# Kernel optimization log

Measured on AMD Instinct MI355X. Metric: run time of the kernel, lower is better.

The kernel has to match this reference:

```python
import jax, jax.numpy as jnp
import numpy as np

B, T, D = 2, 2048, 2048
HQ, HKV, HD = 16, 8, 128
GROUP = HQ // HKV
EPS = 1e-6


def rms_norm(x, scale):
    # qwen3-compatible: compute in fp32
    xf = x.astype(jnp.float32)
    var = jnp.mean(xf * xf, axis=-1, keepdims=True)
    return (xf * jax.lax.rsqrt(var + EPS) * scale).astype(x.dtype)


def apply_rope(x, cos, sin):
    # x: [B,H,T,d]; cos,sin: [T,d]
    d2 = x.shape[-1] // 2
    x1, x2 = x[..., :d2], x[..., d2:]
    rot = jnp.concatenate([-x2, x1], axis=-1)
    return (x * cos[None, None] + rot * sin[None, None]).astype(x.dtype)


def setup_inputs() -> dict:
    key = jax.random.key(0)
    ks = jax.random.split(key, 8)
    x = jax.random.normal(ks[0], (B, T, D), dtype=jnp.float32)
    # causal mask: True where attention is disallowed (j > i)
    mask = jnp.triu(jnp.ones((T, T), dtype=jnp.bool_), k=1)
    # RoPE tables
    inv_freq = 1.0 / (10000.0 ** (np.arange(0, HD, 2, dtype=np.float32) / HD))
    pos = np.arange(T, dtype=np.float32)
    ang = np.outer(pos, inv_freq)  # [T, HD/2]
    ang = np.concatenate([ang, ang], axis=-1)  # [T, HD]
    cos = jnp.asarray(np.cos(ang), dtype=jnp.float32)
    sin = jnp.asarray(np.sin(ang), dtype=jnp.float32)
    s = 0.02
    Wq = jax.random.normal(ks[1], (HQ * HD, D), dtype=jnp.float32) * s
    Wk = jax.random.normal(ks[2], (HKV * HD, D), dtype=jnp.float32) * s
    Wv = jax.random.normal(ks[3], (HKV * HD, D), dtype=jnp.float32) * s
    Wo = jax.random.normal(ks[4], (D, HQ * HD), dtype=jnp.float32) * s
    q_scale = jnp.ones((HD,), dtype=jnp.float32)
    k_scale = jnp.ones((HD,), dtype=jnp.float32)
    return {"x": x, "mask": mask, "cos": cos, "sin": sin,
            "Wq": Wq, "Wk": Wk, "Wv": Wv, "Wo": Wo,
            "q_scale": q_scale, "k_scale": k_scale}


def reference(x, mask, cos, sin, Wq, Wk, Wv, Wo, q_scale, k_scale):
    Bc, Tc, _ = x.shape
    Q = jnp.einsum('btd,ed->bte', x, Wq).reshape(Bc, Tc, HQ, HD).transpose(0, 2, 1, 3)
    K = jnp.einsum('btd,ed->bte', x, Wk).reshape(Bc, Tc, HKV, HD).transpose(0, 2, 1, 3)
    V = jnp.einsum('btd,ed->bte', x, Wv).reshape(Bc, Tc, HKV, HD).transpose(0, 2, 1, 3)
    Q = rms_norm(Q, q_scale)
    K = rms_norm(K, k_scale)
    Q = apply_rope(Q, cos, sin)
    K = apply_rope(K, cos, sin)
    K = jnp.repeat(K, GROUP, axis=1)  # [B,HQ,T,d]
    V = jnp.repeat(V, GROUP, axis=1)
    S = jnp.einsum('bhqd,bhkd->bhqk', Q, K) / jnp.sqrt(jnp.float32(HD))
    S = jnp.where(mask[None, None], -jnp.inf, S)
    P = jax.nn.softmax(S, axis=-1)
    ctx = jnp.einsum('bhqk,bhkd->bhqd', P, V).transpose(0, 2, 1, 3).reshape(Bc, Tc, HQ * HD)
    return jnp.einsum('bte,de->btd', ctx, Wo)
```

## Files before the change

kernel.cpp:

```cpp
#include <hip/hip_runtime.h>
#include <cstdint>
#include <cstddef>

#define B_ 2
#define T_ 2048
#define D_ 2048
#define HQ_ 16
#define HKV_ 8
#define HD_ 128

typedef __attribute__((ext_vector_type(8))) short short8;
typedef __attribute__((ext_vector_type(8))) unsigned short ushort8;
typedef __attribute__((ext_vector_type(4))) float f32x4;
typedef __attribute__((ext_vector_type(2))) unsigned short ushort2v;
typedef __attribute__((ext_vector_type(4))) unsigned short ushort4v;
typedef __attribute__((ext_vector_type(2))) float float2v;
typedef __attribute__((ext_vector_type(4))) float float4v;

__device__ __forceinline__ unsigned short f2bf(float f) {
  unsigned int u = __builtin_bit_cast(unsigned int, f);
  u += 0x7fffu + ((u >> 16) & 1u);
  return (unsigned short)(u >> 16);
}
__device__ __forceinline__ float bf2f(unsigned short h) {
  unsigned int u = ((unsigned int)h) << 16;
  return __builtin_bit_cast(float, u);
}

#if defined(__has_builtin)
#if __has_builtin(__builtin_amdgcn_global_load_lds)
#define HAS_GLL 1
#endif
#endif
#ifndef HAS_GLL
#define HAS_GLL 0
#endif

__device__ __forceinline__ void gll16(const void* g, void* l) {
#if HAS_GLL
  __builtin_amdgcn_global_load_lds((const __attribute__((address_space(1))) void*)g,
                                   (__attribute__((address_space(3))) void*)l, 16, 0, 0);
#else
  *(ushort8*)((char*)l + (threadIdx.x & 63) * 16) = *(const ushort8*)g;
#endif
}

__global__ __launch_bounds__(256) void cast_all(const float* __restrict__ x,
                                                const float* __restrict__ wq,
                                                const float* __restrict__ wk,
                                                const float* __restrict__ wv,
                                                const float* __restrict__ wo,
                                                unsigned short* __restrict__ xb,
                                                unsigned short* __restrict__ wqkv,
                                                unsigned short* __restrict__ wob) {
  int i = (blockIdx.x * 256 + threadIdx.x) * 4;
  if (i >= 20971520) return;
  const float* s;
  unsigned short* d;
  int soff, doff;
  if (i < 8388608)       { s = x;  soff = i;            d = xb;   doff = i; }
  else if (i < 12582912) { s = wq; soff = i - 8388608;  d = wqkv; doff = i - 8388608; }
  else if (i < 14680064) { s = wk; soff = i - 12582912; d = wqkv; doff = i - 8388608; }
  else if (i < 16777216) { s = wv; soff = i - 14680064; d = wqkv; doff = i - 8388608; }
  else                   { s = wo; soff = i - 16777216; d = wob;  doff = i - 16777216; }
  float4v v = *(const float4v*)(s + soff);
  ushort4v o; o.x = f2bf(v.x); o.y = f2bf(v.y); o.z = f2bf(v.z); o.w = f2bf(v.w);
  *(ushort4v*)(d + doff) = o;
}

template<int M, int N, int K, bool BF16_OUT>
__global__ __launch_bounds__(256) void gemm_bt(const unsigned short* __restrict__ A,
                                               const unsigned short* __restrict__ W,
                                               void* __restrict__ Cout) {
  __shared__ __align__(16) unsigned short As[128 * 32];
  __shared__ __align__(16) unsigned short Bs[128 * 32];
  const int tid = threadIdx.x;
  const int lane = tid & 63;
  const int wv = tid >> 6;
  const int g = lane >> 4;
  const int c = lane & 15;
  const int m0 = blockIdx.y * 128;
  const int n0 = blockIdx.x * 128;
  const int wm = (wv >> 1) * 64;
  const int wn = (wv & 1) * 64;

  f32x4 acc[4][4];
  for (int i = 0; i < 4; i++)
    for (int j = 0; j < 4; j++) acc[i][j] = (f32x4)0.0f;

  const int ch0 = wv * 64 + lane;
  const int r0 = ch0 >> 2, cc0 = (ch0 & 3) * 8;
  const int ch1 = 256 + ch0;
  const int r1 = ch1 >> 2, cc1 = (ch1 & 3) * 8;
  unsigned short* ldsA0 = As + (size_t)(wv * 64) * 8;
  unsigned short* ldsA1 = As + (size_t)(256 + wv * 64) * 8;
  unsigned short* ldsB0 = Bs + (size_t)(wv * 64) * 8;
  unsigned short* ldsB1 = Bs + (size_t)(256 + wv * 64) * 8;

  for (int k0 = 0; k0 < K; k0 += 32) {
    __syncthreads();
    gll16(&A[(size_t)(m0 + r0) * K + k0 + cc0], ldsA0);
    gll16(&A[(size_t)(m0 + r1) * K + k0 + cc1], ldsA1);
    gll16(&W[(size_t)(n0 + r0) * K + k0 + cc0], ldsB0);
    gll16(&W[(size_t)(n0 + r1) * K + k0 + cc1], ldsB1);
    __syncthreads();
    short8 a[4], b[4];
    for (int i = 0; i < 4; i++) a[i] = *(const short8*)&As[(wm + i * 16 + c) * 32 + g * 8];
    for (int j = 0; j < 4; j++) b[j] = *(const short8*)&Bs[(wn + j * 16 + c) * 32 + g * 8];
    for (int i = 0; i < 4; i++)
      for (int j = 0; j < 4; j++)
        acc[i][j] = __builtin_amdgcn_mfma_f32_16x16x32_bf16(a[i], b[j], acc[i][j], 0, 0, 0);
  }

  for (int i = 0; i < 4; i++)
    for (int j = 0; j < 4; j++)
      for (int r = 0; r < 4; r++) {
        int row = m0 + wm + i * 16 + g * 4 + r;
        int col = n0 + wn + j * 16 + c;
        if (BF16_OUT)
          ((unsigned short*)Cout)[(size_t)row * N + col] = f2bf(acc[i][j][r]);
        else
          ((float*)Cout)[(size_t)row * N + col] = acc[i][j][r];
      }
}

__global__ __launch_bounds__(256) void qk_norm_rope(const unsigned short* __restrict__ qkv,
                                                    const float* __restrict__ cosT,
                                                    const float* __restrict__ sinT,
                                                    const float* __restrict__ q_scale,
                                                    const float* __restrict__ k_scale,
                                                    unsigned short* __restrict__ Qb,
                                                    unsigned short* __restrict__ Kb) {
  const int tid = threadIdx.x;
  const int lane = tid & 63;
  const int wv = tid >> 6;
  const int row = blockIdx.x;
  const int b = row >> 11;
  const int t = row & 2047;
  const int d0 = lane * 2;

  const float2v cs = *(const float2v*)&cosT[t * 128 + d0];
  const float2v sn = *(const float2v*)&sinT[t * 128 + d0];
  const float2v qsc = *(const float2v*)&q_scale[d0];
  const float2v ksc = *(const float2v*)&k_scale[d0];
  const float sgn = (lane < 32) ? -1.0f : 1.0f;
  const unsigned short* base = qkv + (size_t)row * 4096;

#pragma unroll
  for (int s6 = 0; s6 < 6; s6++) {
    const int slot = wv * 6 + s6;
    const bool isQ = slot < 16;
    const unsigned short* src = base + (isQ ? slot * 128 : 2048 + (slot - 16) * 128);
    ushort2v u = *(const ushort2v*)&src[d0];
    float x0 = bf2f(u.x), x1 = bf2f(u.y);
    float ss = x0 * x0 + x1 * x1;
    ss += __shfl_xor(ss, 1);  ss += __shfl_xor(ss, 2);  ss += __shfl_xor(ss, 4);
    ss += __shfl_xor(ss, 8);  ss += __shfl_xor(ss, 16); ss += __shfl_xor(ss, 32);
    float rinv = rsqrtf(ss * (1.0f / 128.0f) + 1e-6f);
    float2v scv = isQ ? qsc : ksc;
    float xn0 = x0 * rinv * scv.x;
    float xn1 = x1 * rinv * scv.y;
    float o0 = __shfl_xor(xn0, 32);
    float o1 = __shfl_xor(xn1, 32);
    float r0v = xn0 * cs.x + sgn * o0 * sn.x;
    float r1v = xn1 * cs.y + sgn * o1 * sn.y;
    ushort2v out; out.x = f2bf(r0v); out.y = f2bf(r1v);
    unsigned short* dst;
    if (isQ) dst = Qb + ((size_t)(b * HQ_ + slot) * T_ + t) * HD_;
    else     dst = Kb + ((size_t)(b * HKV_ + (slot - 16)) * T_ + t) * HD_;
    *(ushort2v*)&dst[d0] = out;
  }
}

__global__ __launch_bounds__(256) void v_transpose(const unsigned short* __restrict__ qkv,
                                                   unsigned short* __restrict__ Vt) {
  __shared__ unsigned short lds[128 * 65];
  const int tid = threadIdx.x;
  const int blk = blockIdx.x;
  const int tblk = blk & 31;
  const int kv = (blk >> 5) & 7;
  const int b = blk >> 8;
  const int t0 = tblk * 64;
  const int r = tid >> 2;
  const int seg = tid & 3;
  const unsigned short* src = qkv + (size_t)(b * T_ + t0 + r) * 4096 + 3072 + kv * 128;
  for (int i = 0; i < 4; i++) {
    int cc = seg * 32 + i * 8;
    ushort8 v = *(const ushort8*)&src[cc];
    for (int q = 0; q < 8; q++) lds[(cc + q) * 65 + r] = v[q];
  }
  __syncthreads();
  const int cI = tid >> 1;
  const int rs = (tid & 1) * 32;
  unsigned short* dst = Vt + ((size_t)(b * HKV_ + kv) * HD_ + cI) * T_ + t0 + rs;
  const unsigned short* srow = &lds[cI * 65 + rs];
  for (int j = 0; j < 32; j += 4) {
    ushort4v v; v.x = srow[j]; v.y = srow[j + 1]; v.z = srow[j + 2]; v.w = srow[j + 3];
    *(ushort4v*)&dst[j] = v;
  }
}

__global__ __launch_bounds__(256) void attn(const unsigned short* __restrict__ Qb,
                                            const unsigned short* __restrict__ Kb,
                                            const unsigned short* __restrict__ Vt,
                                            unsigned short* __restrict__ ctxb) {
  __shared__ __align__(16) unsigned short Ks[64 * 128];
  __shared__ __align__(16) unsigned short Vs[128 * 64];
  __shared__ __align__(16) unsigned short Ps[4][16 * 72];
  const int tid = threadIdx.x;
  const int lane = tid & 63;
  const int wv = tid >> 6;
  const int g = lane >> 4;
  const int c = lane & 15;

  const int blk = blockIdx.x;
  const int kv = blk & 7;
  const int idx = blk >> 3;
  const int p = idx >> 2;
  const int b = (idx >> 1) & 1;
  const int h = kv * 2 + (idx & 1);

  const unsigned short* Kh = Kb + (size_t)(b * HKV_ + kv) * T_ * HD_;
  const unsigned short* Vh = Vt + (size_t)(b * HKV_ + kv) * HD_ * T_;
  const float scale = 0.08838834764831845f;

  for (int ph = 0; ph < 2; ph++) {
    const int qb = ph ? (31 - p) : p;
    const int nkt = qb + 1;
    const unsigned short* Qh = Qb + ((size_t)(b * HQ_ + h) * T_ + qb * 64 + wv * 16) * HD_;

    short8 aq[4];
#pragma unroll
    for (int dk = 0; dk < 4; dk++) aq[dk] = *(const short8*)&Qh[c * HD_ + dk * 32 + g * 8];

    f32x4 acc[8];
#pragma unroll
    for (int dc = 0; dc < 8; dc++) acc[dc] = (f32x4)0.0f;
    float lp[4] = {0.0f, 0.0f, 0.0f, 0.0f};

    for (int kt = 0; kt < nkt; kt++) {
      __syncthreads();
#pragma unroll
      for (int i = 0; i < 4; i++) {
        const int ch = wv * 256 + i * 64 + lane;
        const int rowK = ch >> 4, ccK = ch & 15;
        const int sK = ccK ^ (rowK & 7);
        gll16(Kh + (size_t)(kt * 64 + rowK) * HD_ + sK * 8,
              Ks + (size_t)(wv * 256 + i * 64) * 8);
        const int rowV = ch >> 3, ccV = ch & 7;
        const int sV = ccV ^ (rowV & 7);
        gll16(Vh + (size_t)rowV * T_ + kt * 64 + sV * 8,
              Vs + (size_t)(wv * 256 + i * 64) * 8);
      }
      __syncthreads();

      f32x4 s[4];
#pragma unroll
      for (int kf = 0; kf < 4; kf++) s[kf] = (f32x4)0.0f;
#pragma unroll
      for (int dk = 0; dk < 4; dk++) {
#pragma unroll
        for (int kf = 0; kf < 4; kf++) {
          short8 bk = *(const short8*)&Ks[(kf * 16 + c) * 128 + ((dk * 4 + g) ^ (c & 7)) * 8];
          s[kf] = __builtin_amdgcn_mfma_f32_16x16x32_bf16(aq[dk], bk, s[kf], 0, 0, 0);
        }
      }

      const bool diag = (kt == nkt - 1);
#pragma unroll
      for (int kf = 0; kf < 4; kf++) {
#pragma unroll
        for (int r = 0; r < 4; r++) {
          float pv = __expf(s[kf][r] * scale);
          if (diag) {
            int key = kt * 64 + kf * 16 + c;
            int rowq = qb * 64 + wv * 16 + g * 4 + r;
            if (key > rowq) pv = 0.0f;
          }
          lp[r] += pv;
          Ps[wv][(g * 4 + r) * 72 + kf * 16 + c] = f2bf(pv);
        }
      }

      short8 ap[2];
      ap[0] = *(const short8*)&Ps[wv][c * 72 + g * 8];
      ap[1] = *(const short8*)&Ps[wv][c * 72 + 32 + g * 8];
#pragma unroll
      for (int dc = 0; dc < 8; dc++) {
#pragma unroll
        for (int kf2 = 0; kf2 < 2; kf2++) {
          short8 bv = *(const short8*)&Vs[(dc * 16 + c) * 64 + ((kf2 * 4 + g) ^ (c & 7)) * 8];
          acc[dc] = __builtin_amdgcn_mfma_f32_16x16x32_bf16(ap[kf2], bv, acc[dc], 0, 0, 0);
        }
      }
    }

#pragma unroll
    for (int r = 0; r < 4; r++) {
      float l = lp[r];
      l += __shfl_xor(l, 1); l += __shfl_xor(l, 2);
      l += __shfl_xor(l, 4); l += __shfl_xor(l, 8);
      float inv = 1.0f / l;
      int row = b * T_ + qb * 64 + wv * 16 + g * 4 + r;
#pragma unroll
      for (int dc = 0; dc < 8; dc++)
        ctxb[(size_t)row * (HQ_ * HD_) + h * HD_ + dc * 16 + c] = f2bf(acc[dc][r] * inv);
    }
  }
}

extern "C" void kernel_launch(void* const* d_in, const int* in_sizes, int n_in,
                              void* d_out, int out_size, void* d_ws, size_t ws_size,
                              hipStream_t stream) {
  const float* x = (const float*)d_in[0];
  const float* cosT = (const float*)d_in[2];
  const float* sinT = (const float*)d_in[3];
  const float* Wq = (const float*)d_in[4];
  const float* Wk = (const float*)d_in[5];
  const float* Wv = (const float*)d_in[6];
  const float* Wo = (const float*)d_in[7];
  const float* q_scale = (const float*)d_in[8];
  const float* k_scale = (const float*)d_in[9];

  char* ws = (char*)d_ws;
  unsigned short* qkv  = (unsigned short*)(ws + 0);
  unsigned short* ctxb = qkv;
  unsigned short* xb   = (unsigned short*)(ws + 33554432);
  unsigned short* wqkv = (unsigned short*)(ws + 50331648);
  unsigned short* wob  = (unsigned short*)(ws + 67108864);
  unsigned short* Qb   = (unsigned short*)(ws + 75497472);
  unsigned short* Kb   = (unsigned short*)(ws + 92274688);
  unsigned short* Vt   = (unsigned short*)(ws + 100663296);

  cast_all<<<20480, 256, 0, stream>>>(x, Wq, Wk, Wv, Wo, xb, wqkv, wob);
  gemm_bt<4096, 4096, 2048, true><<<dim3(32, 32), 256, 0, stream>>>(xb, wqkv, qkv);
  qk_norm_rope<<<4096, 256, 0, stream>>>(qkv, cosT, sinT, q_scale, k_scale, Qb, Kb);
  v_transpose<<<512, 256, 0, stream>>>(qkv, Vt);
  attn<<<512, 256, 0, stream>>>(Qb, Kb, Vt, ctxb);
  gemm_bt<4096, 2048, 2048, false><<<dim3(16, 32), 256, 0, stream>>>(ctxb, wob, d_out);
}
```

Before: 373.5 us.

## Double-buffer attention K/V tiles, fold softmax scale into Q, split-K output GEMM

The attention kernel now double-buffers its K and V LDS tiles, issuing the next tile's global-to-LDS loads before computing on the current one, which removes one barrier per iteration. The 1/sqrt(d) softmax scale is folded into the Q RMS-norm factor so the exp no longer needs a multiply. The output projection GEMM is split two ways along K, and the fp32 partial results are accumulated with global atomic adds after a memset of the output. This doubles the block count of that GEMM to fill more CUs, at the cost of an extra memset, atomic traffic, and LDS use that doubles for the K/V tiles.

```diff
diff --git a/kernel.cpp b/kernel.cpp
--- a/kernel.cpp
+++ b/kernel.cpp
@@ -31,9 +31,15 @@
 #if __has_builtin(__builtin_amdgcn_global_load_lds)
 #define HAS_GLL 1
 #endif
+#if __has_builtin(__builtin_amdgcn_global_atomic_fadd_f32)
+#define HAS_FADD 1
+#endif
 #endif
 #ifndef HAS_GLL
 #define HAS_GLL 0
+#endif
+#ifndef HAS_FADD
+#define HAS_FADD 0
 #endif
 
 __device__ __forceinline__ void gll16(const void* g, void* l) {
@@ -42,6 +48,14 @@
                                    (__attribute__((address_space(3))) void*)l, 16, 0, 0);
 #else
   *(ushort8*)((char*)l + (threadIdx.x & 63) * 16) = *(const ushort8*)g;
+#endif
+}
+
+__device__ __forceinline__ void gatomic_fadd(float* p, float v) {
+#if HAS_FADD
+  __builtin_amdgcn_global_atomic_fadd_f32((__attribute__((address_space(1))) float*)p, v);
+#else
+  atomicAdd(p, v);
 #endif
 }
 
@@ -68,7 +82,7 @@
   *(ushort4v*)(d + doff) = o;
 }
 
-template<int M, int N, int K, bool BF16_OUT>
+template<int M, int N, int K, bool BF16_OUT, int KSPLIT>
 __global__ __launch_bounds__(256) void gemm_bt(const unsigned short* __restrict__ A,
                                                const unsigned short* __restrict__ W,
                                                void* __restrict__ Cout) {
@@ -81,6 +95,7 @@
   const int c = lane & 15;
   const int m0 = blockIdx.y * 128;
   const int n0 = blockIdx.x * 128;
+  const int kz = (KSPLIT > 1) ? blockIdx.z * (K / KSPLIT) : 0;
   const int wm = (wv >> 1) * 64;
   const int wn = (wv & 1) * 64;
 
@@ -97,7 +112,7 @@
   unsigned short* ldsB0 = Bs + (size_t)(wv * 64) * 8;
   unsigned short* ldsB1 = Bs + (size_t)(256 + wv * 64) * 8;
 
-  for (int k0 = 0; k0 < K; k0 += 32) {
+  for (int k0 = kz; k0 < kz + K / KSPLIT; k0 += 32) {
     __syncthreads();
     gll16(&A[(size_t)(m0 + r0) * K + k0 + cc0], ldsA0);
     gll16(&A[(size_t)(m0 + r1) * K + k0 + cc1], ldsA1);
@@ -119,6 +134,8 @@
         int col = n0 + wn + j * 16 + c;
         if (BF16_OUT)
           ((unsigned short*)Cout)[(size_t)row * N + col] = f2bf(acc[i][j][r]);
+        else if (KSPLIT > 1)
+          gatomic_fadd(&((float*)Cout)[(size_t)row * N + col], acc[i][j][r]);
         else
           ((float*)Cout)[(size_t)row * N + col] = acc[i][j][r];
       }
@@ -157,6 +174,7 @@
     ss += __shfl_xor(ss, 1);  ss += __shfl_xor(ss, 2);  ss += __shfl_xor(ss, 4);
     ss += __shfl_xor(ss, 8);  ss += __shfl_xor(ss, 16); ss += __shfl_xor(ss, 32);
     float rinv = rsqrtf(ss * (1.0f / 128.0f) + 1e-6f);
+    if (isQ) rinv *= 0.08838834764831845f;
     float2v scv = isQ ? qsc : ksc;
     float xn0 = x0 * rinv * scv.x;
     float xn1 = x1 * rinv * scv.y;
@@ -204,8 +222,8 @@
                                             const unsigned short* __restrict__ Kb,
                                             const unsigned short* __restrict__ Vt,
                                             unsigned short* __restrict__ ctxb) {
-  __shared__ __align__(16) unsigned short Ks[64 * 128];
-  __shared__ __align__(16) unsigned short Vs[128 * 64];
+  __shared__ __align__(16) unsigned short Ks[2][64 * 128];
+  __shared__ __align__(16) unsigned short Vs[2][128 * 64];
   __shared__ __align__(16) unsigned short Ps[4][16 * 72];
   const int tid = threadIdx.x;
   const int lane = tid & 63;
@@ -222,7 +240,21 @@
 
   const unsigned short* Kh = Kb + (size_t)(b * HKV_ + kv) * T_ * HD_;
   const unsigned short* Vh = Vt + (size_t)(b * HKV_ + kv) * HD_ * T_;
-  const float scale = 0.08838834764831845f;
+
+  auto stage = [&](int kt, int bi) {
+#pragma unroll
+    for (int i = 0; i < 4; i++) {
+      const int ch = wv * 256 + i * 64 + lane;
+      const int rowK = ch >> 4, ccK = ch & 15;
+      const int sK = ccK ^ (rowK & 7);
+      gll16(Kh + (size_t)(kt * 64 + rowK) * HD_ + sK * 8,
+            Ks[bi] + (size_t)(wv * 256 + i * 64) * 8);
+      const int rowV = ch >> 3, ccV = ch & 7;
+      const int sV = ccV ^ (rowV & 7);
+      gll16(Vh + (size_t)rowV * T_ + kt * 64 + sV * 8,
+            Vs[bi] + (size_t)(wv * 256 + i * 64) * 8);
+    }
+  };
 
   for (int ph = 0; ph < 2; ph++) {
     const int qb = ph ? (31 - p) : p;
@@ -238,21 +270,12 @@
     for (int dc = 0; dc < 8; dc++) acc[dc] = (f32x4)0.0f;
     float lp[4] = {0.0f, 0.0f, 0.0f, 0.0f};
 
+    stage(0, 0);
+    __syncthreads();
+
     for (int kt = 0; kt < nkt; kt++) {
-      __syncthreads();
-#pragma unroll
-      for (int i = 0; i < 4; i++) {
-        const int ch = wv * 256 + i * 64 + lane;
-        const int rowK = ch >> 4, ccK = ch & 15;
-        const int sK = ccK ^ (rowK & 7);
-        gll16(Kh + (size_t)(kt * 64 + rowK) * HD_ + sK * 8,
-              Ks + (size_t)(wv * 256 + i * 64) * 8);
-        const int rowV = ch >> 3, ccV = ch & 7;
-        const int sV = ccV ^ (rowV & 7);
-        gll16(Vh + (size_t)rowV * T_ + kt * 64 + sV * 8,
-              Vs + (size_t)(wv * 256 + i * 64) * 8);
-      }
-      __syncthreads();
+      const int cur = kt & 1;
+      if (kt + 1 < nkt) stage(kt + 1, cur ^ 1);
 
       f32x4 s[4];
 #pragma unroll
@@ -261,7 +284,7 @@
       for (int dk = 0; dk < 4; dk++) {
 #pragma unroll
         for (int kf = 0; kf < 4; kf++) {
-          short8 bk = *(const short8*)&Ks[(kf * 16 + c) * 128 + ((dk * 4 + g) ^ (c & 7)) * 8];
+          short8 bk = *(const short8*)&Ks[cur][(kf * 16 + c) * 128 + ((dk * 4 + g) ^ (c & 7)) * 8];
           s[kf] = __builtin_amdgcn_mfma_f32_16x16x32_bf16(aq[dk], bk, s[kf], 0, 0, 0);
         }
       }
@@ -271,7 +294,7 @@
       for (int kf = 0; kf < 4; kf++) {
 #pragma unroll
         for (int r = 0; r < 4; r++) {
-          float pv = __expf(s[kf][r] * scale);
+          float pv = __expf(s[kf][r]);
           if (diag) {
             int key = kt * 64 + kf * 16 + c;
             int rowq = qb * 64 + wv * 16 + g * 4 + r;
@@ -289,10 +312,12 @@
       for (int dc = 0; dc < 8; dc++) {
 #pragma unroll
         for (int kf2 = 0; kf2 < 2; kf2++) {
-          short8 bv = *(const short8*)&Vs[(dc * 16 + c) * 64 + ((kf2 * 4 + g) ^ (c & 7)) * 8];
+          short8 bv = *(const short8*)&Vs[cur][(dc * 16 + c) * 64 + ((kf2 * 4 + g) ^ (c & 7)) * 8];
           acc[dc] = __builtin_amdgcn_mfma_f32_16x16x32_bf16(ap[kf2], bv, acc[dc], 0, 0, 0);
         }
       }
+
+      __syncthreads();
     }
 
 #pragma unroll
@@ -333,9 +358,10 @@
   unsigned short* Vt   = (unsigned short*)(ws + 100663296);
 
   cast_all<<<20480, 256, 0, stream>>>(x, Wq, Wk, Wv, Wo, xb, wqkv, wob);
-  gemm_bt<4096, 4096, 2048, true><<<dim3(32, 32), 256, 0, stream>>>(xb, wqkv, qkv);
+  gemm_bt<4096, 4096, 2048, true, 1><<<dim3(32, 32), 256, 0, stream>>>(xb, wqkv, qkv);
   qk_norm_rope<<<4096, 256, 0, stream>>>(qkv, cosT, sinT, q_scale, k_scale, Qb, Kb);
   v_transpose<<<512, 256, 0, stream>>>(qkv, Vt);
   attn<<<512, 256, 0, stream>>>(Qb, Kb, Vt, ctxb);
-  gemm_bt<4096, 2048, 2048, false><<<dim3(16, 32), 256, 0, stream>>>(ctxb, wob, d_out);
-}
+  hipMemsetAsync(d_out, 0, (size_t)4096 * 2048 * 4, stream);
+  gemm_bt<4096, 2048, 2048, false, 2><<<dim3(16, 32, 2), 256, 0, stream>>>(ctxb, wob, d_out);
+}
```

New measurement: 404.9 us. +8.4%, slower.
